# Kernel tuning notes

Hardware: AMD Instinct MI355X
Metric: run time of the kernel (lower is better)

## Reference

```python
import jax, jax.numpy as jnp
import numpy as np

DIM_IN = 10000
LW = [512, 512]
EW = [16, 16]


def setup_inputs() -> dict:
    key = jax.random.key(0)
    ks = jax.random.split(key, 16)
    x = jax.random.normal(ks[0], (4096, DIM_IN), dtype=jnp.float32)
    mask = jax.random.randint(ks[1], (4096, DIM_IN), 0, 2).astype(jnp.float32)
    s = 0.02
    # LNet: dim_in -> 512 -> 512 -> dim_in (tanh after hidden layers only)
    W1 = jax.random.normal(ks[2], (DIM_IN, LW[0]), dtype=jnp.float32) * s
    b1 = jnp.zeros((LW[0],), jnp.float32)
    W2 = jax.random.normal(ks[3], (LW[0], LW[1]), dtype=jnp.float32) * s
    b2 = jnp.zeros((LW[1],), jnp.float32)
    W3 = jax.random.normal(ks[4], (LW[1], DIM_IN), dtype=jnp.float32) * s
    b3 = jnp.zeros((DIM_IN,), jnp.float32)
    # ENet: 1 -> 16 -> 16 -> 1
    E1w = jax.random.normal(ks[5], (1, EW[0]), dtype=jnp.float32) * s
    E1b = jnp.zeros((EW[0],), jnp.float32)
    E2w = jax.random.normal(ks[6], (EW[0], EW[1]), dtype=jnp.float32) * s
    E2b = jnp.zeros((EW[1],), jnp.float32)
    E3w = jax.random.normal(ks[7], (EW[1], 1), dtype=jnp.float32) * s
    E3b = jnp.zeros((1,), jnp.float32)
    return {"x": x, "mask": mask, "W1": W1, "b1": b1, "W2": W2, "b2": b2,
            "W3": W3, "b3": b3, "E1w": E1w, "E1b": E1b, "E2w": E2w,
            "E2b": E2b, "E3w": E3w, "E3b": E3b}


def reference(x, mask, W1, b1, W2, b2, W3, b3, E1w, E1b, E2w, E2b, E3w, E3b):
    # LNet: two tanh hidden layers + final linear
    h = jnp.tanh(x @ W1 + b1)            # [B, 512]
    h = jnp.tanh(h @ W2 + b2)            # [B, 512]
    out = h @ W3 + b3                    # [B, dim_in]
    # ENet applied elementwise to scalar entries; original gathers x[mask>0],
    # runs ENet, adds 0.8*y residual, scatters back. Equivalent dense form:
    v = out[..., None]                   # [B, dim_in, 1]
    e = jnp.tanh(v @ E1w + E1b)          # [B, dim_in, 16]
    e = jnp.tanh(e @ E2w + E2b)          # [B, dim_in, 16]
    e = (e @ E3w + E3b)[..., 0]          # [B, dim_in]
    y = e + 0.8 * out
    return jnp.where(mask > 0, y, out)
```

## Files before the change

### kernel.cpp

```cpp
#include <hip/hip_runtime.h>
#include <stdint.h>

typedef unsigned short u16;
typedef u16 u16x8 __attribute__((ext_vector_type(8)));
typedef __bf16 bf16x8 __attribute__((ext_vector_type(8)));
typedef float f32x4 __attribute__((ext_vector_type(4)));

__device__ __forceinline__ float b2f(u16 u) {
    union { unsigned int i; float f; } c; c.i = ((unsigned int)u) << 16; return c.f;
}
__device__ __forceinline__ u16 f2b(float f) {
    unsigned int u = __float_as_uint(f);
    u += 0x7fff + ((u >> 16) & 1);
    return (u16)(u >> 16);
}

typedef const __attribute__((address_space(1))) unsigned int* gas_p;
typedef __attribute__((address_space(3))) unsigned int* las_p;
__device__ __forceinline__ void gll16(const void* g, void* l) {
    __builtin_amdgcn_global_load_lds((gas_p)g, (las_p)l, 16, 0, 0);
}

__global__ __launch_bounds__(1024) void detect_dtype(const u16* __restrict__ m,
                                                     int* __restrict__ flag) {
    __shared__ int s;
    int t = threadIdx.x;
    if (t == 0) s = 0;
    __syncthreads();
    if (m[2 * t] != 0) atomicOr(&s, 1);
    __syncthreads();
    if (t == 0) *flag = s;
}

__global__ __launch_bounds__(256) void canon_params(
        const void* b1, const void* b2, const void* b3,
        const void* E1w, const void* E1b, const void* E2w,
        const void* E2b, const void* E3w, const void* E3b,
        const int* __restrict__ flag, float* __restrict__ dst) {
    const int DT = *flag;
    int i = blockIdx.x * 256 + threadIdx.x;
    if (i >= 11345) return;
    const void* srcs[9] = {b1, b2, b3, E1w, E1b, E2w, E2b, E3w, E3b};
    const int off[10] = {0, 512, 1024, 11024, 11040, 11056, 11312, 11328, 11344, 11345};
    int s = 0;
    while (i >= off[s + 1]) ++s;
    int j = i - off[s];
    dst[i] = (DT == 1) ? b2f(((const u16*)srcs[s])[j]) : ((const float*)srcs[s])[j];
}

__global__ __launch_bounds__(256) void transpose_pad(const void* __restrict__ vin,
        u16* __restrict__ out, const int* __restrict__ flag,
        int R, int C, int ldi, int ldo) {
    const int DT = *flag;
    __shared__ __align__(16) u16 tile[64][72];
    const int rt = blockIdx.x * 64;
    const int ct = blockIdx.y * 64;
    const int t = threadIdx.x;
    const int lr = t >> 2;
    const int lc = (t & 3) * 16;
    const int r = rt + lr;
    if (r < R && (ct + lc + 15) < C) {
        if (DT == 1) {
            const u16* p = (const u16*)vin + (long)r * ldi + ct + lc;
            *(u16x8*)&tile[lr][lc]     = *(const u16x8*)p;
            *(u16x8*)&tile[lr][lc + 8] = *(const u16x8*)(p + 8);
        } else {
            const float* p = (const float*)vin + (long)r * ldi + ct + lc;
            #pragma unroll
            for (int q = 0; q < 4; ++q) {
                f32x4 v4 = *(const f32x4*)(p + q * 4);
                #pragma unroll
                for (int j = 0; j < 4; ++j) tile[lr][lc + q * 4 + j] = f2b(v4[j]);
            }
        }
    } else {
        #pragma unroll
        for (int j = 0; j < 16; ++j) {
            int c = ct + lc + j;
            u16 v = 0;
            if (r < R && c < C)
                v = (DT == 1) ? ((const u16*)vin)[(long)r * ldi + c]
                              : f2b(((const float*)vin)[(long)r * ldi + c]);
            tile[lr][lc + j] = v;
        }
    }
    __syncthreads();
    const int oc = ct + lr;
    if (oc >= C) return;
    u16x8 w0, w1;
    #pragma unroll
    for (int j = 0; j < 8; ++j) w0[j] = tile[lc + j][lr];
    #pragma unroll
    for (int j = 0; j < 8; ++j) w1[j] = tile[lc + 8 + j][lr];
    long ob = (long)oc * ldo + rt + lc;
    if (rt + lc + 15 < ldo) {
        *(u16x8*)(out + ob)     = w0;
        *(u16x8*)(out + ob + 8) = w1;
    } else {
        #pragma unroll
        for (int j = 0; j < 16; ++j) {
            int orr = rt + lc + j;
            if (orr < ldo) out[(long)oc * ldo + orr] = (j < 8) ? w0[j] : w1[j - 8];
        }
    }
}

__global__ __launch_bounds__(256) void build_elut(const float* __restrict__ P,
                                                  float* __restrict__ lut) {
    const float* E1w = P + 11024; const float* E1b = P + 11040;
    const float* E2w = P + 11056; const float* E2b = P + 11312;
    const float* E3w = P + 11328; const float* E3b = P + 11344;
    int i = blockIdx.x * 256 + threadIdx.x;
    if (i >= 4096) return;
    float v = -16.f + (float)i * (1.f / 128.f);
    float e1[16];
    #pragma unroll
    for (int j = 0; j < 16; ++j) e1[j] = tanhf(v * E1w[j] + E1b[j]);
    float e = E3b[0];
    #pragma unroll
    for (int k = 0; k < 16; ++k) {
        float s = E2b[k];
        #pragma unroll
        for (int j = 0; j < 16; ++j) s += e1[j] * E2w[j * 16 + k];
        e += tanhf(s) * E3w[k];
    }
    lut[i] = e;
}

template<int MODE, int XDT>
__global__ __launch_bounds__(256, 4) void gemm_bt(
        const void* __restrict__ A, const u16* __restrict__ Bt,
        const float* __restrict__ biasf, void* __restrict__ Cb,
        float* __restrict__ Cf, const void* __restrict__ mask,
        const float* __restrict__ lut, const int* __restrict__ flag,
        int M, int N, int K, int Kloop, int kchunk, int ldA, int ldB, int ldC) {
    if (flag && *flag != XDT) return;
    constexpr int ADT = (MODE == 2) ? XDT : 1;
    constexpr bool GLL = (ADT == 1);

    __shared__ __align__(16) u16 Alds[128 * 32];
    __shared__ __align__(16) u16 Blds[128 * 32];
    __shared__ __align__(16) float lutS[(MODE == 1) ? 4096 : 4];

    const int tid = threadIdx.x;
    const int m0 = blockIdx.x * 128;
    const int n0 = blockIdx.y * 128;
    const int lane = tid & 63;
    const int w = tid >> 6;
    const int wm = (w >> 1) * 64;
    const int wn = (w & 1) * 64;
    const int lm = lane & 15;
    const int lq = lane >> 4;

    if (MODE == 1) {
        const f32x4* s = (const f32x4*)lut;
        f32x4* d = (f32x4*)lutS;
        #pragma unroll
        for (int i = 0; i < 4; ++i) d[tid + 256 * i] = s[tid + 256 * i];
    }

    const int arow = tid >> 2;
    const int kq8 = (((tid & 3) ^ (arow & 3))) * 8;
    const long aoff = (long)(m0 + arow) * ldA + kq8;
    const long boff = (long)(n0 + arow) * ldB + kq8;
    u16* aldst0 = &Alds[tid * 8];
    u16* aldst1 = &Alds[tid * 8 + 2048];
    u16* bldst0 = &Blds[tid * 8];
    u16* bldst1 = &Blds[tid * 8 + 2048];
    const bool bv0 = (n0 + arow) < N;
    const bool bv1 = (n0 + arow + 64) < N;

    const int sx = (lq ^ (lm & 3)) * 8;
    const u16* aB = &Alds[(wm + lm) * 32 + sx];
    const u16* bB = &Blds[(wn + lm) * 32 + sx];

    const f32x4 zero = {0.f, 0.f, 0.f, 0.f};
    const u16x8 z8 = {0, 0, 0, 0, 0, 0, 0, 0};
    f32x4 acc[4][4];
    #pragma unroll
    for (int i = 0; i < 4; ++i)
        #pragma unroll
        for (int j = 0; j < 4; ++j) acc[i][j] = zero;

    int kb = 0, ke = Kloop;
    if (MODE == 2) { kb = blockIdx.z * kchunk; ke = min(Kloop, kb + kchunk); }

    const u16* Au16 = (const u16*)A;

    for (int k0 = kb; k0 < ke; k0 += 32) {
        if (GLL && (k0 + 32 <= K)) {
            __syncthreads();
            gll16(Au16 + aoff + k0, aldst0);
            gll16(Au16 + aoff + 64 * (long)ldA + k0, aldst1);
            gll16(Bt + boff + k0, bldst0);
            gll16(Bt + boff + 64 * (long)ldB + k0, bldst1);
            __syncthreads();
        } else {
            const bool av = (k0 + kq8) < K;
            u16x8 ra0 = z8, ra1 = z8;
            if (ADT == 1) {
                if (av) {
                    ra0 = *(const u16x8*)(Au16 + aoff + k0);
                    ra1 = *(const u16x8*)(Au16 + aoff + 64 * (long)ldA + k0);
                }
            } else {
                const float* Af = (const float*)A;
                if (av) {
                    f32x4 l0 = *(const f32x4*)(Af + aoff + k0);
                    f32x4 h0 = *(const f32x4*)(Af + aoff + k0 + 4);
                    f32x4 l1 = *(const f32x4*)(Af + aoff + 64 * (long)ldA + k0);
                    f32x4 h1 = *(const f32x4*)(Af + aoff + 64 * (long)ldA + k0 + 4);
                    #pragma unroll
                    for (int j = 0; j < 4; ++j) {
                        ra0[j] = f2b(l0[j]); ra0[4 + j] = f2b(h0[j]);
                        ra1[j] = f2b(l1[j]); ra1[4 + j] = f2b(h1[j]);
                    }
                }
            }
            u16x8 rb0 = bv0 ? *(const u16x8*)(Bt + boff + k0) : z8;
            u16x8 rb1 = bv1 ? *(const u16x8*)(Bt + boff + 64 * (long)ldB + k0) : z8;
            __syncthreads();
            *(u16x8*)aldst0 = ra0;
            *(u16x8*)aldst1 = ra1;
            *(u16x8*)bldst0 = rb0;
            *(u16x8*)bldst1 = rb1;
            __syncthreads();
        }
        bf16x8 a[4], b[4];
        #pragma unroll
        for (int i = 0; i < 4; ++i) a[i] = *(const bf16x8*)(aB + i * 512);
        #pragma unroll
        for (int i = 0; i < 4; ++i) b[i] = *(const bf16x8*)(bB + i * 512);
        #pragma unroll
        for (int mi = 0; mi < 4; ++mi)
            #pragma unroll
            for (int ni = 0; ni < 4; ++ni)
                acc[mi][ni] = __builtin_amdgcn_mfma_f32_16x16x32_bf16(
                    a[mi], b[ni], acc[mi][ni], 0, 0, 0);
    }

    if (MODE == 2) {
        float* dst = Cf + (long)blockIdx.z * M * (long)N;
        #pragma unroll
        for (int mi = 0; mi < 4; ++mi) {
            const int row0 = m0 + wm + mi * 16 + lq * 4;
            #pragma unroll
            for (int ni = 0; ni < 4; ++ni) {
                const int col = n0 + wn + ni * 16 + lm;
                #pragma unroll
                for (int r = 0; r < 4; ++r)
                    dst[(long)(row0 + r) * ldC + col] = acc[mi][ni][r];
            }
        }
    } else if (MODE == 0) {
        #pragma unroll
        for (int mi = 0; mi < 4; ++mi) {
            const int row0 = m0 + wm + mi * 16 + lq * 4;
            #pragma unroll
            for (int ni = 0; ni < 4; ++ni) {
                const int col = n0 + wn + ni * 16 + lm;
                const float bc = biasf[col];
                #pragma unroll
                for (int r = 0; r < 4; ++r) {
                    float v = acc[mi][ni][r] + bc;
                    ((u16*)Cb)[(long)(row0 + r) * ldC + col] = f2b(tanhf(v));
                }
            }
        }
    } else {
        #pragma unroll
        for (int mi = 0; mi < 4; ++mi) {
            const int row0 = m0 + wm + mi * 16 + lq * 4;
            #pragma unroll
            for (int ni = 0; ni < 4; ++ni) {
                const int col = n0 + wn + ni * 16 + lm;
                if (col < N) {
                    const float bc = biasf[col];
                    #pragma unroll
                    for (int r = 0; r < 4; ++r) {
                        float v = acc[mi][ni][r] + bc;
                        float fi = (v + 16.f) * 128.f + 0.5f;
                        int idx = (int)fi;
                        idx = idx < 0 ? 0 : (idx > 4095 ? 4095 : idx);
                        float y = lutS[idx] + 0.8f * v;
                        long off = (long)(row0 + r) * ldC + col;
                        float mk = (XDT == 1) ? b2f(((const u16*)mask)[off])
                                              : ((const float*)mask)[off];
                        float res = mk > 0.f ? y : v;
                        if (XDT == 1) ((u16*)Cb)[off] = f2b(res);
                        else          ((float*)Cb)[off] = res;
                    }
                }
            }
        }
    }
}

__global__ __launch_bounds__(256) void reduce_tanh8(const float* __restrict__ p,
        const float* __restrict__ biasf, u16* __restrict__ h, int MN) {
    int i = (blockIdx.x * 256 + threadIdx.x) * 4;
    if (i >= MN) return;
    f32x4 s = *(const f32x4*)(p + i);
    #pragma unroll
    for (int z = 1; z < 8; ++z) s += *(const f32x4*)(p + (long)z * MN + i);
    int col = i & 511;
    #pragma unroll
    for (int c = 0; c < 4; ++c)
        h[i + c] = f2b(tanhf(s[c] + biasf[col + c]));
}

extern "C" void kernel_launch(void* const* d_in, const int* in_sizes, int n_in,
                              void* d_out, int out_size, void* d_ws, size_t ws_size,
                              hipStream_t stream) {
    const void* x    = d_in[0];
    const void* mask = d_in[1];
    const void* W1   = d_in[2];
    const void* b1   = d_in[3];
    const void* W2   = d_in[4];
    const void* b2   = d_in[5];
    const void* W3   = d_in[6];
    const void* b3   = d_in[7];

    const int B = 4096, D = 10000, H = 512, KP = 10016;

    char* ob = (char*)d_out;
    u16*   W1T     = (u16*)ob;
    float* partial = (float*)(ob + 10256384);
    u16*   h1      = (u16*)(ob + 77365248);
    u16*   W2T     = (u16*)(ob + 10256384);

    char* ws = (char*)d_ws;
    u16*   W3T   = (u16*)ws;
    u16*   h2    = (u16*)(ws + 10240000);
    float* elut  = (float*)(ws + 14434304);
    int*   flag  = (int*)(ws + 14450688);
    float* canon = (float*)(ws + 14450704);
    float* b1f = canon, * b2f = canon + 512, * b3f = canon + 1024;

    detect_dtype<<<1, 1024, 0, stream>>>((const u16*)mask, flag);

    canon_params<<<45, 256, 0, stream>>>(b1, b2, b3, d_in[8], d_in[9],
        d_in[10], d_in[11], d_in[12], d_in[13], flag, canon);

    transpose_pad<<<dim3(157, 8), 256, 0, stream>>>(W1, W1T, flag, D, H, H, KP);
    transpose_pad<<<dim3(8, 157), 256, 0, stream>>>(W3, W3T, flag, H, D, D, H);

    build_elut<<<16, 256, 0, stream>>>(canon, elut);

    gemm_bt<2, 0><<<dim3(32, 4, 8), 256, 0, stream>>>(x, W1T, nullptr, nullptr,
        partial, nullptr, nullptr, flag, B, H, D, KP, 1280, D, KP, H);
    gemm_bt<2, 1><<<dim3(32, 4, 8), 256, 0, stream>>>(x, W1T, nullptr, nullptr,
        partial, nullptr, nullptr, flag, B, H, D, KP, 1280, D, KP, H);
    reduce_tanh8<<<(B * H) / 1024, 256, 0, stream>>>(partial, b1f, h1, B * H);

    transpose_pad<<<dim3(8, 8), 256, 0, stream>>>(W2, W2T, flag, H, H, H, H);

    gemm_bt<0, 1><<<dim3(32, 4), 256, 0, stream>>>(h1, W2T, b2f, h2, nullptr,
        nullptr, nullptr, nullptr, B, H, H, H, 0, H, H, H);

    gemm_bt<1, 0><<<dim3(32, 79), 256, 0, stream>>>(h2, W3T, b3f, d_out, nullptr,
        mask, elut, flag, B, D, H, H, 0, H, H, D);
    gemm_bt<1, 1><<<dim3(32, 79), 256, 0, stream>>>(h2, W3T, b3f, d_out, nullptr,
        mask, elut, flag, B, D, H, H, 0, H, H, D);
}
```

Before: 624.9 us.

## Double-buffer LDS tiles with async global-to-LDS loads and adjust swizzle

Splits the shared-memory A/B tiles into two buffers so the global_load_lds for the next K-step is issued before the MFMA compute on the current tile. This removes one barrier per iteration and lets load latency overlap with matrix math. It also changes the XOR swizzle to use row bits 1-2 to reduce LDS bank conflicts. LDS use doubles, which may lower occupancy under launch_bounds(256,4). The non-GLL tail path is kept as a register-staged step.

Result: slower. 672.6 us (+7.6%).

```diff
diff --git a/kernel.cpp b/kernel.cpp
--- a/kernel.cpp
+++ b/kernel.cpp
@@ -138,8 +138,10 @@
     constexpr int ADT = (MODE == 2) ? XDT : 1;
     constexpr bool GLL = (ADT == 1);
 
-    __shared__ __align__(16) u16 Alds[128 * 32];
-    __shared__ __align__(16) u16 Blds[128 * 32];
+    __shared__ __align__(16) u16 A0s[128 * 32];
+    __shared__ __align__(16) u16 B0s[128 * 32];
+    __shared__ __align__(16) u16 A1s[128 * 32];
+    __shared__ __align__(16) u16 B1s[128 * 32];
     __shared__ __align__(16) float lutS[(MODE == 1) ? 4096 : 4];
 
     const int tid = threadIdx.x;
@@ -160,19 +162,13 @@
     }
 
     const int arow = tid >> 2;
-    const int kq8 = (((tid & 3) ^ (arow & 3))) * 8;
+    const int kq8 = ((tid & 3) ^ ((arow >> 1) & 3)) * 8;
     const long aoff = (long)(m0 + arow) * ldA + kq8;
     const long boff = (long)(n0 + arow) * ldB + kq8;
-    u16* aldst0 = &Alds[tid * 8];
-    u16* aldst1 = &Alds[tid * 8 + 2048];
-    u16* bldst0 = &Blds[tid * 8];
-    u16* bldst1 = &Blds[tid * 8 + 2048];
     const bool bv0 = (n0 + arow) < N;
     const bool bv1 = (n0 + arow + 64) < N;
 
-    const int sx = (lq ^ (lm & 3)) * 8;
-    const u16* aB = &Alds[(wm + lm) * 32 + sx];
-    const u16* bB = &Blds[(wn + lm) * 32 + sx];
+    const int sx = (lq ^ ((lm >> 1) & 3)) * 8;
 
     const f32x4 zero = {0.f, 0.f, 0.f, 0.f};
     const u16x8 z8 = {0, 0, 0, 0, 0, 0, 0, 0};
@@ -187,57 +183,90 @@
 
     const u16* Au16 = (const u16*)A;
 
-    for (int k0 = kb; k0 < ke; k0 += 32) {
-        if (GLL && (k0 + 32 <= K)) {
+#define STAGE(As, Bs, kk) do {                                                \
+        gll16(Au16 + aoff + (kk), &(As)[tid * 8]);                            \
+        gll16(Au16 + aoff + 64 * (long)ldA + (kk), &(As)[tid * 8 + 2048]);    \
+        gll16(Bt + boff + (kk), &(Bs)[tid * 8]);                              \
+        gll16(Bt + boff + 64 * (long)ldB + (kk), &(Bs)[tid * 8 + 2048]);      \
+    } while (0)
+
+#define COMPUTE(As, Bs) do {                                                  \
+        bf16x8 a_[4], b_[4];                                                  \
+        const u16* ab_ = &(As)[(wm + lm) * 32 + sx];                          \
+        const u16* bb_ = &(Bs)[(wn + lm) * 32 + sx];                          \
+        _Pragma("unroll")                                                     \
+        for (int i = 0; i < 4; ++i) a_[i] = *(const bf16x8*)(ab_ + i * 512);  \
+        _Pragma("unroll")                                                     \
+        for (int i = 0; i < 4; ++i) b_[i] = *(const bf16x8*)(bb_ + i * 512);  \
+        _Pragma("unroll")                                                     \
+        for (int mi = 0; mi < 4; ++mi)                                        \
+            _Pragma("unroll")                                                 \
+            for (int ni = 0; ni < 4; ++ni)                                    \
+                acc[mi][ni] = __builtin_amdgcn_mfma_f32_16x16x32_bf16(        \
+                    a_[mi], b_[ni], acc[mi][ni], 0, 0, 0);                    \
+    } while (0)
+
+#define REGSTEP(k0) do {                                                      \
+        const bool av = ((k0) + kq8) < K;                                     \
+        u16x8 ra0 = z8, ra1 = z8;                                             \
+        if (ADT == 1) {                                                       \
+            if (av) {                                                         \
+                ra0 = *(const u16x8*)(Au16 + aoff + (k0));                    \
+                ra1 = *(const u16x8*)(Au16 + aoff + 64 * (long)ldA + (k0));   \
+            }                                                                 \
+        } else {                                                              \
+            const float* Af = (const float*)A;                                \
+            if (av) {                                                         \
+                f32x4 l0 = *(const f32x4*)(Af + aoff + (k0));                 \
+                f32x4 h0 = *(const f32x4*)(Af + aoff + (k0) + 4);             \
+                f32x4 l1 = *(const f32x4*)(Af + aoff + 64 * (long)ldA + (k0));\
+                f32x4 h1 = *(const f32x4*)(Af + aoff + 64 * (long)ldA + (k0) + 4);\
+                _Pragma("unroll")                                             \
+                for (int j = 0; j < 4; ++j) {                                 \
+                    ra0[j] = f2b(l0[j]); ra0[4 + j] = f2b(h0[j]);             \
+                    ra1[j] = f2b(l1[j]); ra1[4 + j] = f2b(h1[j]);             \
+                }                                                             \
+            }                                                                 \
+        }                                                                     \
+        u16x8 rb0 = bv0 ? *(const u16x8*)(Bt + boff + (k0)) : z8;             \
+        u16x8 rb1 = bv1 ? *(const u16x8*)(Bt + boff + 64 * (long)ldB + (k0)) : z8;\
+        __syncthreads();                                                      \
+        *(u16x8*)&A0s[tid * 8] = ra0;                                         \
+        *(u16x8*)&A0s[tid * 8 + 2048] = ra1;                                  \
+        *(u16x8*)&B0s[tid * 8] = rb0;                                         \
+        *(u16x8*)&B0s[tid * 8 + 2048] = rb1;                                  \
+        __syncthreads();                                                      \
+        COMPUTE(A0s, B0s);                                                    \
+    } while (0)
+
+    if (GLL) {
+        int total = (ke - kb + 31) >> 5;
+        int nf = (K - kb) >> 5;
+        if (nf > total) nf = total;
+        const int kfe = kb + (nf << 5);
+        if (nf > 0) {
+            STAGE(A0s, B0s, kb);
             __syncthreads();
-            gll16(Au16 + aoff + k0, aldst0);
-            gll16(Au16 + aoff + 64 * (long)ldA + k0, aldst1);
-            gll16(Bt + boff + k0, bldst0);
-            gll16(Bt + boff + 64 * (long)ldB + k0, bldst1);
-            __syncthreads();
-        } else {
-            const bool av = (k0 + kq8) < K;
-            u16x8 ra0 = z8, ra1 = z8;
-            if (ADT == 1) {
-                if (av) {
-                    ra0 = *(const u16x8*)(Au16 + aoff + k0);
-                    ra1 = *(const u16x8*)(Au16 + aoff + 64 * (long)ldA + k0);
+            for (int i = 0; i < nf; ++i) {
+                const int tn = kb + ((i + 1) << 5);
+                if ((i & 1) == 0) {
+                    if (i + 1 < nf) STAGE(A1s, B1s, tn);
+                    COMPUTE(A0s, B0s);
+                } else {
+                    if (i + 1 < nf) STAGE(A0s, B0s, tn);
+                    COMPUTE(A1s, B1s);
                 }
-            } else {
-                const float* Af = (const float*)A;
-                if (av) {
-                    f32x4 l0 = *(const f32x4*)(Af + aoff + k0);
-                    f32x4 h0 = *(const f32x4*)(Af + aoff + k0 + 4);
-                    f32x4 l1 = *(const f32x4*)(Af + aoff + 64 * (long)ldA + k0);
-                    f32x4 h1 = *(const f32x4*)(Af + aoff + 64 * (long)ldA + k0 + 4);
-                    #pragma unroll
-                    for (int j = 0; j < 4; ++j) {
-                        ra0[j] = f2b(l0[j]); ra0[4 + j] = f2b(h0[j]);
-                        ra1[j] = f2b(l1[j]); ra1[4 + j] = f2b(h1[j]);
-                    }
-                }
-            }
-            u16x8 rb0 = bv0 ? *(const u16x8*)(Bt + boff + k0) : z8;
-            u16x8 rb1 = bv1 ? *(const u16x8*)(Bt + boff + 64 * (long)ldB + k0) : z8;
-            __syncthreads();
-            *(u16x8*)aldst0 = ra0;
-            *(u16x8*)aldst1 = ra1;
-            *(u16x8*)bldst0 = rb0;
-            *(u16x8*)bldst1 = rb1;
-            __syncthreads();
-        }
-        bf16x8 a[4], b[4];
-        #pragma unroll
-        for (int i = 0; i < 4; ++i) a[i] = *(const bf16x8*)(aB + i * 512);
-        #pragma unroll
-        for (int i = 0; i < 4; ++i) b[i] = *(const bf16x8*)(bB + i * 512);
-        #pragma unroll
-        for (int mi = 0; mi < 4; ++mi)
-            #pragma unroll
-            for (int ni = 0; ni < 4; ++ni)
-                acc[mi][ni] = __builtin_amdgcn_mfma_f32_16x16x32_bf16(
-                    a[mi], b[ni], acc[mi][ni], 0, 0, 0);
-    }
+                __syncthreads();
+            }
+        }
+        for (int k0 = kfe; k0 < ke; k0 += 32) REGSTEP(k0);
+    } else {
+        for (int k0 = kb; k0 < ke; k0 += 32) REGSTEP(k0);
+    }
+
+#undef STAGE
+#undef COMPUTE
+#undef REGSTEP
 
     if (MODE == 2) {
         float* dst = Cf + (long)blockIdx.z * M * (long)N;
```
